# Optimization experiments

Hardware: AMD Instinct MI355X
Metric: run time of the kernel (lower is better)

Reference implementation:

```python
import jax, jax.numpy as jnp
import numpy as np

EMBEDDING_DIM = 512
HEAD_DIM = 64
B, T_NEW, T_CACHE = 8, 1024, 3072
T_TOTAL = T_NEW + T_CACHE


def setup_inputs() -> dict:
    key = jax.random.key(0)
    ks = jax.random.split(key, 6)
    x = jax.random.normal(ks[0], (B, T_NEW, EMBEDDING_DIM), dtype=jnp.float32)
    cache_k = jax.random.normal(ks[1], (B, T_CACHE, HEAD_DIM), dtype=jnp.float32)
    cache_v = jax.random.normal(ks[2], (B, T_CACHE, HEAD_DIM), dtype=jnp.float32)
    # Causal mask rows for the new tokens: cache fully visible, causal among new.
    # Equivalent to tril(ones(T_TOTAL, T_TOTAL))[T_CACHE:, :].
    rows = jnp.arange(T_NEW)[:, None] + T_CACHE  # absolute positions of new tokens
    cols = jnp.arange(T_TOTAL)[None, :]
    mask = (cols <= rows).astype(jnp.int32)  # [T_NEW, T_TOTAL]
    scale = 1.0 / np.sqrt(EMBEDDING_DIM)
    Wq = jax.random.normal(ks[3], (EMBEDDING_DIM, HEAD_DIM), dtype=jnp.float32) * scale
    Wk = jax.random.normal(ks[4], (EMBEDDING_DIM, HEAD_DIM), dtype=jnp.float32) * scale
    Wv = jax.random.normal(ks[5], (EMBEDDING_DIM, HEAD_DIM), dtype=jnp.float32) * scale
    return {"x": x, "mask": mask, "cache_k": cache_k, "cache_v": cache_v,
            "Wq": Wq, "Wk": Wk, "Wv": Wv}


def reference(x, mask, cache_k, cache_v, Wq, Wk, Wv):
    # Projections (nn.Linear with bias=False)
    q = jnp.einsum("btc,cd->btd", x, Wq)  # [B, T_new, D]
    k_new = jnp.einsum("btc,cd->btd", x, Wk)
    v_new = jnp.einsum("btc,cd->btd", x, Wv)
    k = jnp.concatenate([cache_k, k_new], axis=1)  # [B, T_total, D]
    v = jnp.concatenate([cache_v, v_new], axis=1)
    d = k.shape[-1]
    scores = jnp.einsum("btd,bsd->bts", q, k) * (d ** -0.5)  # [B, T_new, T_total]
    T = q.shape[1]
    cur_mask = mask[:T, :k.shape[1]]  # [T_new, T_total]
    scores = jnp.where(cur_mask == 0, jnp.float32(-jnp.inf), scores)
    probs = jax.nn.softmax(scores, axis=-1)
    # Dropout is identity in eval mode (deterministic reference).
    out = jnp.einsum("bts,bsd->btd", probs, v)  # [B, T_new, D]
    return out, k, v
```

## Files before the change

kernel.cpp:

```cpp
#include <hip/hip_runtime.h>

#define NB     8
#define TNEW   1024
#define TCACHE 3072
#define TTOT   4096
#define EMB    512
#define HD     64

typedef __bf16 bf16x8 __attribute__((ext_vector_type(8)));
typedef __bf16 bf16x4 __attribute__((ext_vector_type(4)));
typedef float  f32x4  __attribute__((ext_vector_type(4)));

#define MFMA(a,b,c) __builtin_amdgcn_mfma_f32_16x16x32_bf16((a),(b),(c),0,0,0)

#define GLOAD_LDS16(g, l) \
    __builtin_amdgcn_global_load_lds((const __attribute__((address_space(1))) void*)(g), \
                                     (__attribute__((address_space(3))) void*)(l), 16, 0, 0)

#define QSCALE 0.180336880f

#define WS_WT   0
#define WS_KBF  196608
#define WS_VTB  4390912
#define WS_OP   8585216
#define WS_ML   16973824


__global__ __launch_bounds__(256) void prep(const float* __restrict__ ck,
                                            const float* __restrict__ cv,
                                            const float* __restrict__ Wq,
                                            const float* __restrict__ Wk,
                                            const float* __restrict__ Wv,
                                            float* __restrict__ kout,
                                            float* __restrict__ vout,
                                            __bf16* __restrict__ kb,
                                            __bf16* __restrict__ vtb,
                                            __bf16* __restrict__ wt) {
    __shared__ __bf16 vl[64][72];
    const int blk = blockIdx.x;
    const int tid = threadIdx.x;
    if (blk < 768) {
#pragma unroll
        for (int it = 0; it < 2; ++it) {
            const int i = blk * 256 + tid + it * 196608;
            const int b = i / 49152;
            const int f = i - b * 49152;
            const int s = f >> 4, d = (f & 15) * 4;
            const float4 kd = ((const float4*)ck)[i];
            ((float4*)(kout + (size_t)b * TTOT * HD))[f] = kd;
            bf16x4 k4;
            k4[0] = (__bf16)kd.x; k4[1] = (__bf16)kd.y;
            k4[2] = (__bf16)kd.z; k4[3] = (__bf16)kd.w;
            *(bf16x4*)(kb + (size_t)b * TTOT * HD + s * HD + d) = k4;
        }
    } else if (blk < 1152) {
        const int tb = blk - 768;
        const int b = tb / 48, si = tb - (tb / 48) * 48;
        const int sbase = si * 64;
        const float4* src = (const float4*)(cv + ((size_t)b * TCACHE + sbase) * HD);
        float4* dstf = (float4*)(vout + ((size_t)b * TTOT + sbase) * HD);
#pragma unroll
        for (int k = 0; k < 4; ++k) {
            const int f = tid + 256 * k;
            const int s = f >> 4, d4 = (f & 15) * 4;
            const float4 v = src[f];
            dstf[f] = v;
            bf16x4 t;
            t[0] = (__bf16)v.x; t[1] = (__bf16)v.y;
            t[2] = (__bf16)v.z; t[3] = (__bf16)v.w;
            *(bf16x4*)&vl[s][d4] = t;
        }
        __syncthreads();
        const int d = tid >> 2, sc = tid & 3;
        bf16x8 o0, o1;
#pragma unroll
        for (int i = 0; i < 8; ++i) {
            o0[i] = vl[sc * 16 + i][d];
            o1[i] = vl[sc * 16 + 8 + i][d];
        }
        __bf16* vt = vtb + ((size_t)b * HD + d) * TTOT + sbase + sc * 16;
        *(bf16x8*)vt = o0;
        *(bf16x8*)(vt + 8) = o1;
    } else {
        const int tb = blk - 1152;
        const int m = tb >> 3;
        const int ct = (tb & 7) * 64;
        const float* W = (m == 0) ? Wq : (m == 1) ? Wk : Wv;
        const float4* src = (const float4*)(W + (size_t)ct * HD);
#pragma unroll
        for (int k = 0; k < 4; ++k) {
            const int f = tid + 256 * k;
            const int c = f >> 4, d4 = (f & 15) * 4;
            const float4 v = src[f];
            bf16x4 t;
            t[0] = (__bf16)v.x; t[1] = (__bf16)v.y;
            t[2] = (__bf16)v.z; t[3] = (__bf16)v.w;
            *(bf16x4*)&vl[c][d4] = t;
        }
        __syncthreads();
        const int d = tid >> 2, sc = tid & 3;
        bf16x8 o0, o1;
#pragma unroll
        for (int i = 0; i < 8; ++i) {
            o0[i] = vl[sc * 16 + i][d];
            o1[i] = vl[sc * 16 + 8 + i][d];
        }
        __bf16* wr = wt + (size_t)m * HD * EMB + (size_t)d * EMB + ct + sc * 16;
        *(bf16x8*)wr = o0;
        *(bf16x8*)(wr + 8) = o1;
    }
}

__global__ __launch_bounds__(128) void proj_mfma(const float* __restrict__ x,
                                                 const __bf16* __restrict__ wt,
                                                 __bf16* __restrict__ qb,
                                                 float* __restrict__ kout,
                                                 float* __restrict__ vout,
                                                 __bf16* __restrict__ kb,
                                                 __bf16* __restrict__ vtb) {
    __shared__ __bf16 xs[32][520];
    __shared__ __bf16 vls[2][64][24];
    const int tid = threadIdx.x;
    const int w = tid >> 6, lane = tid & 63;
    const int lo = lane & 15, hi = lane >> 4;
    const int r0 = blockIdx.x * 32 + w * 16;
    const int b = r0 >> 10;
    const int t0r = r0 & (TNEW - 1);

    {
        const float4* xg = (const float4*)(x + (size_t)blockIdx.x * 32 * EMB);
#pragma unroll
        for (int k = 0; k < 32; ++k) {
            const int f = tid + 128 * k;
            const int row = f >> 7, col4 = (f & 127) * 4;
            const float4 v = xg[f];
            bf16x4 t;
            t[0] = (__bf16)v.x; t[1] = (__bf16)v.y;
            t[2] = (__bf16)v.z; t[3] = (__bf16)v.w;
            *(bf16x4*)&xs[row][col4] = t;
        }
    }
    __syncthreads();

    for (int m = 0; m < 3; ++m) {
        const __bf16* wm = wt + (size_t)m * HD * EMB;
        f32x4 acc[4];
#pragma unroll
        for (int n = 0; n < 4; ++n) acc[n] = (f32x4){0.f, 0.f, 0.f, 0.f};
#pragma unroll
        for (int c = 0; c < 16; ++c) {
            const bf16x8 ax = *(const bf16x8*)&xs[w * 16 + lo][c * 32 + hi * 8];
#pragma unroll
            for (int n = 0; n < 4; ++n) {
                const bf16x8 bw = *(const bf16x8*)(wm + (size_t)(n * 16 + lo) * EMB + c * 32 + hi * 8);
                acc[n] = MFMA(ax, bw, acc[n]);
            }
        }
#pragma unroll
        for (int n = 0; n < 4; ++n) {
#pragma unroll
            for (int rr = 0; rr < 4; ++rr) {
                const int grow = r0 + hi * 4 + rr;
                const int t = grow & (TNEW - 1);
                const int d = n * 16 + lo;
                const float val = acc[n][rr];
                if (m == 0) {
                    qb[(size_t)grow * HD + d] = (__bf16)(val * QSCALE);
                } else if (m == 1) {
                    const size_t kv = ((size_t)b * TTOT + TCACHE + t) * HD + d;
                    kout[kv] = val;
                    kb[kv] = (__bf16)val;
                } else {
                    const size_t kv = ((size_t)b * TTOT + TCACHE + t) * HD + d;
                    vout[kv] = val;
                    vls[w][d][hi * 4 + rr] = (__bf16)val;
                }
            }
        }
    }
    __syncthreads();
    bf16x8 v0 = *(const bf16x8*)&vls[w][lane][0];
    bf16x8 v1 = *(const bf16x8*)&vls[w][lane][8];
    __bf16* vt = vtb + ((size_t)b * HD + lane) * TTOT + TCACHE + t0r;
    *(bf16x8*)vt = v0;
    *(bf16x8*)(vt + 8) = v1;
}

#define QB 128
#define NSPLIT 8
__global__ __launch_bounds__(512, 4) void attn_mfma(const __bf16* __restrict__ qb,
                                                    const __bf16* __restrict__ kb,
                                                    const __bf16* __restrict__ vtb,
                                                    __bf16* __restrict__ Opart,
                                                    float* __restrict__ mlpart) {
    __shared__ __align__(16) __bf16 Kt[2][64 * 64];
    __shared__ __align__(16) __bf16 Vts[2][64 * 64];
    __shared__ __align__(16) __bf16 P_lds[8][16][72];

    const int tid = threadIdx.x;
    const int wv = tid >> 6, lane = tid & 63;
    const int lo = lane & 15, hi = lane >> 4;

    const int bid = blockIdx.x;
    const int b = bid & 7;
    const int idx = bid >> 3;
    const int split = idx & 7;
    const int qloc = idx >> 3;
    const int t0 = qloc * QB;
    const int row0 = b * TNEW + t0;

    const int ntiles = (TCACHE + t0 + QB) >> 6;
    const int count = (ntiles - split + 7) >> 3;

    const __bf16* Kb = kb + (size_t)b * TTOT * HD;
    const __bf16* Vb = vtb + (size_t)b * HD * TTOT;

    const int r_sub = lane >> 3;
    const int row_st = wv * 8 + r_sub;
    const int c_st = ((lane & 7) * 16) ^ (r_sub << 4);

    const int t0w = t0 + wv * 16;
    const __bf16* Qw = qb + (size_t)(row0 + wv * 16) * HD;
    const bf16x8 aq0 = *(const bf16x8*)(Qw + (size_t)lo * HD + hi * 8);
    const bf16x8 aq1 = *(const bf16x8*)(Qw + (size_t)lo * HD + 32 + hi * 8);

    f32x4 o[4];
    float mg = -1e30f, lg = 0.f;
#pragma unroll
    for (int n = 0; n < 4; ++n) o[n] = (f32x4){0.f, 0.f, 0.f, 0.f};

    {
        const int s0 = split * 64;
        const char* gk = (const char*)Kb + (size_t)(s0 + row_st) * 128 + c_st;
        const char* gv = (const char*)Vb + ((size_t)row_st * TTOT + s0) * 2 + c_st;
        GLOAD_LDS16(gk, Kt[0] + row_st * 64);
        GLOAD_LDS16(gv, Vts[0] + row_st * 64);
    }
    __syncthreads();

    const int sw = (lo & 7) << 3;

    int s0 = split * 64;
    for (int it = 0; it < count; ++it, s0 += NSPLIT * 64) {
        const int buf = it & 1;
        if (it + 1 < count) {
            const int sn = s0 + NSPLIT * 64;
            const char* gk = (const char*)Kb + (size_t)(sn + row_st) * 128 + c_st;
            const char* gv = (const char*)Vb + ((size_t)row_st * TTOT + sn) * 2 + c_st;
            GLOAD_LDS16(gk, Kt[buf ^ 1] + row_st * 64);
            GLOAD_LDS16(gv, Vts[buf ^ 1] + row_st * 64);
        }

        const __bf16* Kl = Kt[buf];
        const __bf16* Vl = Vts[buf];

        bf16x8 bk[4][2], bv[4][2];
#pragma unroll
        for (int kg = 0; kg < 4; ++kg) {
            const int kr = (kg * 16 + lo) * 64;
            bk[kg][0] = *(const bf16x8*)(Kl + kr + ((hi * 8) ^ sw));
            bk[kg][1] = *(const bf16x8*)(Kl + kr + ((32 + hi * 8) ^ sw));
        }
#pragma unroll
        for (int n = 0; n < 4; ++n) {
            const int vr = (n * 16 + lo) * 64;
            bv[n][0] = *(const bf16x8*)(Vl + vr + ((hi * 8) ^ sw));
            bv[n][1] = *(const bf16x8*)(Vl + vr + ((32 + hi * 8) ^ sw));
        }

        const f32x4 z = (f32x4){0.f, 0.f, 0.f, 0.f};
        f32x4 sc[4];
#pragma unroll
        for (int kg = 0; kg < 4; ++kg) {
            sc[kg] = MFMA(bk[kg][0], aq0, z);
            sc[kg] = MFMA(bk[kg][1], aq1, sc[kg]);
        }

        if (s0 + 63 > TCACHE + t0w) {
            const int lim = TCACHE + t0w + lo;
#pragma unroll
            for (int kg = 0; kg < 4; ++kg)
#pragma unroll
                for (int rr = 0; rr < 4; ++rr)
                    if (s0 + kg * 16 + hi * 4 + rr > lim) sc[kg][rr] = -1e30f;
        }

        f32x4 mx = sc[0];
        mx = (f32x4){fmaxf(mx[0], sc[1][0]), fmaxf(mx[1], sc[1][1]),
                     fmaxf(mx[2], sc[1][2]), fmaxf(mx[3], sc[1][3])};
        mx = (f32x4){fmaxf(mx[0], sc[2][0]), fmaxf(mx[1], sc[2][1]),
                     fmaxf(mx[2], sc[2][2]), fmaxf(mx[3], sc[2][3])};
        mx = (f32x4){fmaxf(mx[0], sc[3][0]), fmaxf(mx[1], sc[3][1]),
                     fmaxf(mx[2], sc[3][2]), fmaxf(mx[3], sc[3][3])};
        float mt = fmaxf(fmaxf(mx[0], mx[1]), fmaxf(mx[2], mx[3]));
        mt = fmaxf(mt, __shfl_xor(mt, 16));
        mt = fmaxf(mt, __shfl_xor(mt, 32));

        if (__any(mt > mg + 8.0f)) {
            const float mn = fmaxf(mg, mt);
            const float corr = exp2f(mg - mn);
            lg *= corr;
            mg = mn;
            float cb[4];
#pragma unroll
            for (int rr = 0; rr < 4; ++rr) cb[rr] = __shfl(corr, hi * 4 + rr);
#pragma unroll
            for (int n = 0; n < 4; ++n)
#pragma unroll
                for (int rr = 0; rr < 4; ++rr) o[n][rr] *= cb[rr];
        }

        float ps = 0.f;
#pragma unroll
        for (int kg = 0; kg < 4; ++kg) {
            const float e0 = exp2f(sc[kg][0] - mg);
            const float e1 = exp2f(sc[kg][1] - mg);
            const float e2 = exp2f(sc[kg][2] - mg);
            const float e3 = exp2f(sc[kg][3] - mg);
            ps += (e0 + e1) + (e2 + e3);
            bf16x4 pk;
            pk[0] = (__bf16)e0; pk[1] = (__bf16)e1;
            pk[2] = (__bf16)e2; pk[3] = (__bf16)e3;
            *(bf16x4*)&P_lds[wv][lo][kg * 16 + hi * 4] = pk;
        }
        ps += __shfl_xor(ps, 16);
        ps += __shfl_xor(ps, 32);
        lg += ps;
        asm volatile("" ::: "memory");

        const bf16x8 ap0 = *(const bf16x8*)&P_lds[wv][lo][hi * 8];
        const bf16x8 ap1 = *(const bf16x8*)&P_lds[wv][lo][32 + hi * 8];
#pragma unroll
        for (int n = 0; n < 4; ++n) o[n] = MFMA(ap0, bv[n][0], o[n]);
#pragma unroll
        for (int n = 0; n < 4; ++n) o[n] = MFMA(ap1, bv[n][1], o[n]);
        asm volatile("" ::: "memory");

        __syncthreads();
    }

    __bf16* Ow = Opart + ((size_t)split * (NB * TNEW) + row0 + wv * 16) * HD;
#pragma unroll
    for (int n = 0; n < 4; ++n)
#pragma unroll
        for (int rr = 0; rr < 4; ++rr)
            Ow[(size_t)(hi * 4 + rr) * HD + n * 16 + lo] = (__bf16)o[n][rr];
    if (hi == 0) {
        float* mlw = mlpart + ((size_t)split * (NB * TNEW) + row0 + wv * 16) * 2;
        mlw[lo * 2]     = mg;
        mlw[lo * 2 + 1] = lg;
    }
}

__global__ __launch_bounds__(256) void combine(const __bf16* __restrict__ Opart,
                                               const float* __restrict__ mlpart,
                                               float* __restrict__ out) {
    const int e = blockIdx.x * 256 + threadIdx.x;
    const int lane = threadIdx.x & 63;
    const int row = e >> 6, d = e & 63;
    const float2 ml2 = *(const float2*)&mlpart[(((size_t)(lane & 7)) * (NB * TNEW) + row) * 2];
    float mf = -1e30f;
#pragma unroll
    for (int s = 0; s < NSPLIT; ++s) mf = fmaxf(mf, __shfl(ml2.x, s));
    float lf = 0.f, acc = 0.f;
#pragma unroll
    for (int s = 0; s < NSPLIT; ++s) {
        const float ms = __shfl(ml2.x, s);
        const float ls = __shfl(ml2.y, s);
        const float f = exp2f(ms - mf);
        lf += ls * f;
        acc += (float)Opart[((size_t)s * (NB * TNEW) + row) * HD + d] * f;
    }
    out[e] = acc / lf;
}

extern "C" void kernel_launch(void* const* d_in, const int* in_sizes, int n_in,
                              void* d_out, int out_size, void* d_ws, size_t ws_size,
                              hipStream_t stream) {
    (void)in_sizes; (void)n_in; (void)out_size; (void)ws_size;
    const float* x  = (const float*)d_in[0];
    const float* ck = (const float*)d_in[2];
    const float* cv = (const float*)d_in[3];
    const float* Wq = (const float*)d_in[4];
    const float* Wk = (const float*)d_in[5];
    const float* Wv = (const float*)d_in[6];

    float* out  = (float*)d_out;
    float* kout = out + (size_t)NB * TNEW * HD;
    float* vout = kout + (size_t)NB * TTOT * HD;

    char* ws = (char*)d_ws;
    __bf16* wt  = (__bf16*)(ws + WS_WT);
    __bf16* kbf = (__bf16*)(ws + WS_KBF);
    __bf16* vtb = (__bf16*)(ws + WS_VTB);
    __bf16* Op  = (__bf16*)(ws + WS_OP);
    float*  ml  = (float*)(ws + WS_ML);
    __bf16* qb  = (__bf16*)d_out;

    prep<<<dim3(1176), dim3(256), 0, stream>>>(ck, cv, Wq, Wk, Wv, kout, vout, kbf, vtb, wt);
    proj_mfma<<<dim3(256), dim3(128), 0, stream>>>(x, wt, qb, kout, vout, kbf, vtb);
    attn_mfma<<<dim3(512), dim3(512), 0, stream>>>(qb, kbf, vtb, Op, ml);
    combine<<<dim3(2048), dim3(256), 0, stream>>>(Op, ml, out);
}
```

Before: 51.17 us.

## Use single-wave attention blocks loading K/V directly from global memory

Replaces the 8-wave attention block, which shared double-buffered K/V tiles in LDS via global_load_lds, with 4096 single-wave blocks that each handle 16 query rows and load K and V fragments straight from global memory into registers. This removes the LDS staging, the block-wide barriers and the tile prefetch. In exchange, each K/V tile is now fetched by every wave rather than shared across 8 waves, which raises global/L2 traffic eightfold and leaves load latency unhidden by any explicit prefetch.

```diff
diff --git a/kernel.cpp b/kernel.cpp
--- a/kernel.cpp
+++ b/kernel.cpp
@@ -12,10 +12,6 @@
 typedef float  f32x4  __attribute__((ext_vector_type(4)));
 
 #define MFMA(a,b,c) __builtin_amdgcn_mfma_f32_16x16x32_bf16((a),(b),(c),0,0,0)
-
-#define GLOAD_LDS16(g, l) \
-    __builtin_amdgcn_global_load_lds((const __attribute__((address_space(1))) void*)(g), \
-                                     (__attribute__((address_space(3))) void*)(l), 16, 0, 0)
 
 #define QSCALE 0.180336880f
 
@@ -186,41 +182,32 @@
     *(bf16x8*)(vt + 8) = v1;
 }
 
-#define QB 128
 #define NSPLIT 8
-__global__ __launch_bounds__(512, 4) void attn_mfma(const __bf16* __restrict__ qb,
-                                                    const __bf16* __restrict__ kb,
-                                                    const __bf16* __restrict__ vtb,
-                                                    __bf16* __restrict__ Opart,
-                                                    float* __restrict__ mlpart) {
-    __shared__ __align__(16) __bf16 Kt[2][64 * 64];
-    __shared__ __align__(16) __bf16 Vts[2][64 * 64];
-    __shared__ __align__(16) __bf16 P_lds[8][16][72];
-
-    const int tid = threadIdx.x;
-    const int wv = tid >> 6, lane = tid & 63;
+__global__ __launch_bounds__(64, 4) void attn_mfma(const __bf16* __restrict__ qb,
+                                                   const __bf16* __restrict__ kb,
+                                                   const __bf16* __restrict__ vtb,
+                                                   __bf16* __restrict__ Opart,
+                                                   float* __restrict__ mlpart) {
+    __shared__ __align__(16) __bf16 P_lds[16][72];
+
+    const int lane = threadIdx.x;
     const int lo = lane & 15, hi = lane >> 4;
 
     const int bid = blockIdx.x;
     const int b = bid & 7;
-    const int idx = bid >> 3;
-    const int split = idx & 7;
-    const int qloc = idx >> 3;
-    const int t0 = qloc * QB;
-    const int row0 = b * TNEW + t0;
-
-    const int ntiles = (TCACHE + t0 + QB) >> 6;
-    const int count = (ntiles - split + 7) >> 3;
+    const int rest = bid >> 3;
+    const int split = rest & 7;
+    const int rg = rest >> 3;
+    const int t0w = rg * 16;
+    const int row0 = b * TNEW + t0w;
+
+    const int ntiles = (TCACHE + t0w + 16) >> 6;
+    const int count = (ntiles - split + NSPLIT - 1) >> 3;
 
     const __bf16* Kb = kb + (size_t)b * TTOT * HD;
     const __bf16* Vb = vtb + (size_t)b * HD * TTOT;
 
-    const int r_sub = lane >> 3;
-    const int row_st = wv * 8 + r_sub;
-    const int c_st = ((lane & 7) * 16) ^ (r_sub << 4);
-
-    const int t0w = t0 + wv * 16;
-    const __bf16* Qw = qb + (size_t)(row0 + wv * 16) * HD;
+    const __bf16* Qw = qb + (size_t)row0 * HD;
     const bf16x8 aq0 = *(const bf16x8*)(Qw + (size_t)lo * HD + hi * 8);
     const bf16x8 aq1 = *(const bf16x8*)(Qw + (size_t)lo * HD + 32 + hi * 8);
 
@@ -229,43 +216,14 @@
 #pragma unroll
     for (int n = 0; n < 4; ++n) o[n] = (f32x4){0.f, 0.f, 0.f, 0.f};
 
-    {
-        const int s0 = split * 64;
-        const char* gk = (const char*)Kb + (size_t)(s0 + row_st) * 128 + c_st;
-        const char* gv = (const char*)Vb + ((size_t)row_st * TTOT + s0) * 2 + c_st;
-        GLOAD_LDS16(gk, Kt[0] + row_st * 64);
-        GLOAD_LDS16(gv, Vts[0] + row_st * 64);
-    }
-    __syncthreads();
-
-    const int sw = (lo & 7) << 3;
-
     int s0 = split * 64;
     for (int it = 0; it < count; ++it, s0 += NSPLIT * 64) {
-        const int buf = it & 1;
-        if (it + 1 < count) {
-            const int sn = s0 + NSPLIT * 64;
-            const char* gk = (const char*)Kb + (size_t)(sn + row_st) * 128 + c_st;
-            const char* gv = (const char*)Vb + ((size_t)row_st * TTOT + sn) * 2 + c_st;
-            GLOAD_LDS16(gk, Kt[buf ^ 1] + row_st * 64);
-            GLOAD_LDS16(gv, Vts[buf ^ 1] + row_st * 64);
-        }
-
-        const __bf16* Kl = Kt[buf];
-        const __bf16* Vl = Vts[buf];
-
-        bf16x8 bk[4][2], bv[4][2];
+        bf16x8 bk[4][2];
 #pragma unroll
         for (int kg = 0; kg < 4; ++kg) {
-            const int kr = (kg * 16 + lo) * 64;
-            bk[kg][0] = *(const bf16x8*)(Kl + kr + ((hi * 8) ^ sw));
-            bk[kg][1] = *(const bf16x8*)(Kl + kr + ((32 + hi * 8) ^ sw));
-        }
-#pragma unroll
-        for (int n = 0; n < 4; ++n) {
-            const int vr = (n * 16 + lo) * 64;
-            bv[n][0] = *(const bf16x8*)(Vl + vr + ((hi * 8) ^ sw));
-            bv[n][1] = *(const bf16x8*)(Vl + vr + ((32 + hi * 8) ^ sw));
+            const __bf16* kr = Kb + (size_t)(s0 + kg * 16 + lo) * HD + hi * 8;
+            bk[kg][0] = *(const bf16x8*)kr;
+            bk[kg][1] = *(const bf16x8*)(kr + 32);
         }
 
         const f32x4 z = (f32x4){0.f, 0.f, 0.f, 0.f};
@@ -274,6 +232,14 @@
         for (int kg = 0; kg < 4; ++kg) {
             sc[kg] = MFMA(bk[kg][0], aq0, z);
             sc[kg] = MFMA(bk[kg][1], aq1, sc[kg]);
+        }
+
+        bf16x8 bv[4][2];
+#pragma unroll
+        for (int n = 0; n < 4; ++n) {
+            const __bf16* vr = Vb + (size_t)(n * 16 + lo) * TTOT + s0 + hi * 8;
+            bv[n][0] = *(const bf16x8*)vr;
+            bv[n][1] = *(const bf16x8*)(vr + 32);
         }
 
         if (s0 + 63 > TCACHE + t0w) {
@@ -321,32 +287,30 @@
             bf16x4 pk;
             pk[0] = (__bf16)e0; pk[1] = (__bf16)e1;
             pk[2] = (__bf16)e2; pk[3] = (__bf16)e3;
-            *(bf16x4*)&P_lds[wv][lo][kg * 16 + hi * 4] = pk;
+            *(bf16x4*)&P_lds[lo][kg * 16 + hi * 4] = pk;
         }
         ps += __shfl_xor(ps, 16);
         ps += __shfl_xor(ps, 32);
         lg += ps;
         asm volatile("" ::: "memory");
 
-        const bf16x8 ap0 = *(const bf16x8*)&P_lds[wv][lo][hi * 8];
-        const bf16x8 ap1 = *(const bf16x8*)&P_lds[wv][lo][32 + hi * 8];
+        const bf16x8 ap0 = *(const bf16x8*)&P_lds[lo][hi * 8];
+        const bf16x8 ap1 = *(const bf16x8*)&P_lds[lo][32 + hi * 8];
 #pragma unroll
         for (int n = 0; n < 4; ++n) o[n] = MFMA(ap0, bv[n][0], o[n]);
 #pragma unroll
         for (int n = 0; n < 4; ++n) o[n] = MFMA(ap1, bv[n][1], o[n]);
         asm volatile("" ::: "memory");
-
-        __syncthreads();
-    }
-
-    __bf16* Ow = Opart + ((size_t)split * (NB * TNEW) + row0 + wv * 16) * HD;
+    }
+
+    __bf16* Ow = Opart + ((size_t)split * (NB * TNEW) + row0) * HD;
 #pragma unroll
     for (int n = 0; n < 4; ++n)
 #pragma unroll
         for (int rr = 0; rr < 4; ++rr)
             Ow[(size_t)(hi * 4 + rr) * HD + n * 16 + lo] = (__bf16)o[n][rr];
     if (hi == 0) {
-        float* mlw = mlpart + ((size_t)split * (NB * TNEW) + row0 + wv * 16) * 2;
+        float* mlw = mlpart + ((size_t)split * (NB * TNEW) + row0) * 2;
         mlw[lo * 2]     = mg;
         mlw[lo * 2 + 1] = lg;
     }
@@ -399,6 +363,6 @@
 
     prep<<<dim3(1176), dim3(256), 0, stream>>>(ck, cv, Wq, Wk, Wv, kout, vout, kbf, vtb, wt);
     proj_mfma<<<dim3(256), dim3(128), 0, stream>>>(x, wt, qb, kout, vout, kbf, vtb);
-    attn_mfma<<<dim3(512), dim3(512), 0, stream>>>(qb, kbf, vtb, Op, ml);
+    attn_mfma<<<dim3(4096), dim3(64), 0, stream>>>(qb, kbf, vtb, Op, ml);
     combine<<<dim3(2048), dim3(256), 0, stream>>>(Op, ml, out);
 }
```

Result: slower. 87.96 us (+71.9%).

## Triple-buffer K/V tiles with explicit vmcnt waits in attention loop

Applied to the files above, without the earlier changes.

Moves the K/V LDS staging from double to triple buffering, so loads are issued two iterations ahead. The full __syncthreads is replaced by s_waitcnt vmcnt(2) plus a raw s_barrier, which waits only for the older tile and leaves the newest load in flight. The aim is to hide global-to-LDS latency better in the attention kernel. In exchange, LDS use grows by 16 KB per block, which may reduce occupancy under launch_bounds(512,4). Correctness now depends on the hand-counted vmcnt values.

```diff
diff --git a/kernel.cpp b/kernel.cpp
--- a/kernel.cpp
+++ b/kernel.cpp
@@ -193,8 +193,8 @@
                                                     const __bf16* __restrict__ vtb,
                                                     __bf16* __restrict__ Opart,
                                                     float* __restrict__ mlpart) {
-    __shared__ __align__(16) __bf16 Kt[2][64 * 64];
-    __shared__ __align__(16) __bf16 Vts[2][64 * 64];
+    __shared__ __align__(16) __bf16 Kt[3][64 * 64];
+    __shared__ __align__(16) __bf16 Vts[3][64 * 64];
     __shared__ __align__(16) __bf16 P_lds[8][16][72];
 
     const int tid = threadIdx.x;
@@ -219,6 +219,13 @@
     const int row_st = wv * 8 + r_sub;
     const int c_st = ((lane & 7) * 16) ^ (r_sub << 4);
 
+#define STAGE(s, bi) do { \
+        const char* gk_ = (const char*)Kb + (size_t)((s) + row_st) * 128 + c_st; \
+        const char* gv_ = (const char*)Vb + ((size_t)row_st * TTOT + (s)) * 2 + c_st; \
+        GLOAD_LDS16(gk_, Kt[bi] + row_st * 64); \
+        GLOAD_LDS16(gv_, Vts[bi] + row_st * 64); \
+    } while (0)
+
     const int t0w = t0 + wv * 16;
     const __bf16* Qw = qb + (size_t)(row0 + wv * 16) * HD;
     const bf16x8 aq0 = *(const bf16x8*)(Qw + (size_t)lo * HD + hi * 8);
@@ -229,28 +236,21 @@
 #pragma unroll
     for (int n = 0; n < 4; ++n) o[n] = (f32x4){0.f, 0.f, 0.f, 0.f};
 
-    {
-        const int s0 = split * 64;
-        const char* gk = (const char*)Kb + (size_t)(s0 + row_st) * 128 + c_st;
-        const char* gv = (const char*)Vb + ((size_t)row_st * TTOT + s0) * 2 + c_st;
-        GLOAD_LDS16(gk, Kt[0] + row_st * 64);
-        GLOAD_LDS16(gv, Vts[0] + row_st * 64);
-    }
-    __syncthreads();
+    STAGE(split * 64, 0);
+    if (count > 1) {
+        STAGE(split * 64 + 512, 1);
+        asm volatile("s_waitcnt vmcnt(2)" ::: "memory");
+    } else {
+        asm volatile("s_waitcnt vmcnt(0)" ::: "memory");
+    }
+    __builtin_amdgcn_s_barrier();
+    __builtin_amdgcn_sched_barrier(0);
 
     const int sw = (lo & 7) << 3;
 
     int s0 = split * 64;
+    int buf = 0;
     for (int it = 0; it < count; ++it, s0 += NSPLIT * 64) {
-        const int buf = it & 1;
-        if (it + 1 < count) {
-            const int sn = s0 + NSPLIT * 64;
-            const char* gk = (const char*)Kb + (size_t)(sn + row_st) * 128 + c_st;
-            const char* gv = (const char*)Vb + ((size_t)row_st * TTOT + sn) * 2 + c_st;
-            GLOAD_LDS16(gk, Kt[buf ^ 1] + row_st * 64);
-            GLOAD_LDS16(gv, Vts[buf ^ 1] + row_st * 64);
-        }
-
         const __bf16* Kl = Kt[buf];
         const __bf16* Vl = Vts[buf];
 
@@ -336,8 +336,19 @@
         for (int n = 0; n < 4; ++n) o[n] = MFMA(ap1, bv[n][1], o[n]);
         asm volatile("" ::: "memory");
 
-        __syncthreads();
-    }
+        if (it + 2 < count) {
+            int nb = buf + 2; if (nb >= 3) nb -= 3;
+            STAGE(s0 + 2 * NSPLIT * 64, nb);
+        }
+        if (it + 1 < count) {
+            if (it + 2 < count) { asm volatile("s_waitcnt vmcnt(2)" ::: "memory"); }
+            else                { asm volatile("s_waitcnt vmcnt(0)" ::: "memory"); }
+            __builtin_amdgcn_s_barrier();
+            __builtin_amdgcn_sched_barrier(0);
+        }
+        buf = (buf == 2) ? 0 : buf + 1;
+    }
+#undef STAGE
 
     __bf16* Ow = Opart + ((size_t)split * (NB * TNEW) + row0 + wv * 16) * HD;
 #pragma unroll
```

Measured after the change: 50.09 us (median of 3 runs). -2.1%, faster.
